# Kernel optimization log

Measured on AMD Instinct MI355X. Metric: run time of the kernel, lower is better.

## Reference

```python
import jax, jax.numpy as jnp
import numpy as np

TAU = 2.0
BN_EPS = 1e-5
SG_ALPHA = 4.0
ATTN_SCALE = 0.125
NUM_HEADS = 8
T, B, C, H, W = 2, 16, 256, 64, 64


@jax.custom_vjp
def heaviside(x):
    return (x >= 0.0).astype(x.dtype)

def _hv_fwd(x):
    return (x >= 0.0).astype(x.dtype), x

def _hv_bwd(x, g):
    s = jax.nn.sigmoid(SG_ALPHA * x)
    return (g * SG_ALPHA * s * (1.0 - s),)

heaviside.defvjp(_hv_fwd, _hv_bwd)


def lif(x_seq, v_th):
    # MultiStepLIFNode: v <- v + (x - v)/tau ; spike = H(v - v_th); hard reset to 0 (detached)
    def step(v, x):
        v = v + (x - v) / TAU
        s = heaviside(v - v_th)
        v = v * (1.0 - jax.lax.stop_gradient(s))
        return v, s
    _, spikes = jax.lax.scan(step, jnp.zeros_like(x_seq[0]), x_seq)
    return spikes


def bn1d(x, gamma, beta, mean, var):
    # eval-mode BatchNorm1d over channel axis 2 of [T,B,C,N]
    inv = (gamma / jnp.sqrt(var + BN_EPS)).reshape(1, 1, -1, 1)
    shift = (beta - mean * gamma / jnp.sqrt(var + BN_EPS)).reshape(1, 1, -1, 1)
    return x * inv + shift


def to_heads(t):
    # [T,B,C,N] -> [T,B,h,N,d]
    t_, b_, c_, n_ = t.shape
    d = c_ // NUM_HEADS
    return t.transpose(0, 1, 3, 2).reshape(t_, b_, n_, NUM_HEADS, d).transpose(0, 1, 3, 2, 4)


def setup_inputs() -> dict:
    key = jax.random.key(0)
    ks = jax.random.split(key, 24)
    w_scale = 0.06  # ~1/sqrt(C)
    inp = {
        'x': jax.random.normal(ks[0], (T, B, C, H, W), jnp.float32),
        'wq': jax.random.normal(ks[1], (C, C), jnp.float32) * w_scale,
        'wk': jax.random.normal(ks[2], (C, C), jnp.float32) * w_scale,
        'wv': jax.random.normal(ks[3], (C, C), jnp.float32) * w_scale,
        'wp': jax.random.normal(ks[4], (C, C), jnp.float32) * w_scale,
        'bp': jax.random.normal(ks[5], (C,), jnp.float32) * 0.1,
    }
    i = 6
    for p in ('q', 'k', 'v', 'p'):
        inp[p + '_gamma'] = jax.random.uniform(ks[i], (C,), jnp.float32, 0.5, 1.5); i += 1
        inp[p + '_beta'] = jax.random.normal(ks[i], (C,), jnp.float32) * 0.1; i += 1
        inp[p + '_mean'] = jax.random.normal(ks[i], (C,), jnp.float32) * 0.1; i += 1
        inp[p + '_var'] = jax.random.uniform(ks[i], (C,), jnp.float32, 0.5, 1.5); i += 1
    return inp


def reference(x, wq, wk, wv, wp, bp,
              q_gamma, q_beta, q_mean, q_var,
              k_gamma, k_beta, k_mean, k_var,
              v_gamma, v_beta, v_mean, v_var,
              p_gamma, p_beta, p_mean, p_var):
    t_, b_, c_, h_, w_ = x.shape
    n_ = h_ * w_
    xs = lif(x, 1.0).reshape(t_, b_, c_, n_)  # proj_lif then flatten(3)
    # 1x1 conv == channel matmul, then BN, then LIF (binary spikes)
    q_out = lif(bn1d(jnp.einsum('oc,tbcn->tbon', wq, xs), q_gamma, q_beta, q_mean, q_var), 1.0)
    k_out = lif(bn1d(jnp.einsum('oc,tbcn->tbon', wk, xs), k_gamma, k_beta, k_mean, k_var), 1.0)
    v_out = lif(bn1d(jnp.einsum('oc,tbcn->tbon', wv, xs), v_gamma, v_beta, v_mean, v_var), 1.0)
    q = to_heads(q_out)
    k = to_heads(k_out)
    v = to_heads(v_out)
    # linear attention: (k^T @ v) then q @ (k^T v)
    kv = jnp.einsum('tbhnd,tbhne->tbhde', k, v)  # [T,B,h,d,d]
    attn = jnp.einsum('tbhnd,tbhde->tbhne', q, kv) * ATTN_SCALE
    attn = attn.transpose(0, 1, 2, 4, 3).reshape(t_, b_, c_, n_)
    s = lif(attn, 0.5)  # attn_lif with v_threshold=0.5
    out = jnp.einsum('oc,tbcn->tbon', wp, s) + bp.reshape(1, 1, -1, 1)
    out = bn1d(out, p_gamma, p_beta, p_mean, p_var).reshape(t_, b_, c_, h_, w_)
    return (out, xs, q_out, k_out, v_out)
```

## Files before the change

### kernel.cpp

```cpp
#include <hip/hip_runtime.h>
#include <cstdint>
#include <cstddef>

typedef __attribute__((ext_vector_type(8))) short short8;
typedef __attribute__((ext_vector_type(4))) float floatx4;
typedef __attribute__((ext_vector_type(4))) unsigned int uintx4;

#define DEV static __device__ __forceinline__

constexpr int NT = 2, NB = 16, NC = 256, NN = 4096, NHD = 8;
constexpr size_t NE1 = (size_t)NT * NB * NC * NN;
constexpr size_t TSTRIDE = (size_t)NB * NC * NN;

DEV unsigned short f2bf(float x) {
  unsigned int u = __builtin_bit_cast(unsigned int, x);
  unsigned int lsb = (u >> 16) & 1u;
  u += 0x7FFFu + lsb;
  return (unsigned short)(u >> 16);
}
DEV float bfb2f(unsigned short h) {
  unsigned int u = ((unsigned int)h) << 16;
  return __builtin_bit_cast(float, u);
}
DEV unsigned int pk2(unsigned short a, unsigned short b) {
  return (unsigned int)a | ((unsigned int)b << 16);
}
DEV int swz(int fr, int kk) { return fr * 4 + (kk ^ ((fr >> 1) & 3)); }
typedef __attribute__((address_space(3))) unsigned int lds_u32;
typedef __attribute__((address_space(1))) const unsigned int glb_u32;
DEV void gld_lds16(const void* g, void* l) {
  __builtin_amdgcn_global_load_lds((glb_u32*)g, (lds_u32*)l, 16, 0, 0);
}

__global__ __launch_bounds__(256) void prep_kernel(
    const float* __restrict__ wq, const float* __restrict__ wk, const float* __restrict__ wv,
    const float* __restrict__ wp, const float* __restrict__ bp,
    const float* __restrict__ qg, const float* __restrict__ qb, const float* __restrict__ qm, const float* __restrict__ qva,
    const float* __restrict__ kg, const float* __restrict__ kb, const float* __restrict__ km, const float* __restrict__ kva,
    const float* __restrict__ vg, const float* __restrict__ vb, const float* __restrict__ vm, const float* __restrict__ vva,
    const float* __restrict__ pg, const float* __restrict__ pb, const float* __restrict__ pm, const float* __restrict__ pva,
    unsigned short* __restrict__ Wqkv, unsigned short* __restrict__ Wp,
    float* __restrict__ invqkv, float* __restrict__ shqkv,
    float* __restrict__ invp, float* __restrict__ shp)
{
  int idx = blockIdx.x * 256 + threadIdx.x;
  if (idx < 196608) {
    int o = idx >> 8, c = idx & 255;
    const float* src = (o < 256) ? wq : (o < 512) ? wk : wv;
    float w = src[(size_t)(o & 255) * 256 + c];
    unsigned short h0 = f2bf(w);  float f0 = bfb2f(h0);
    float r1 = w - f0;
    unsigned short h1 = f2bf(r1); float f1 = bfb2f(h1);
    float r2 = r1 - f1;
    unsigned short h2 = f2bf(r2);
    Wqkv[idx] = h0; Wqkv[196608 + idx] = h1; Wqkv[393216 + idx] = h2;
  } else if (idx < 262144) {
    int j = idx - 196608;
    float w = wp[j];
    unsigned short h0 = f2bf(w);  float f0 = bfb2f(h0);
    float r1 = w - f0;
    unsigned short h1 = f2bf(r1); float f1 = bfb2f(h1);
    float r2 = r1 - f1;
    unsigned short h2 = f2bf(r2);
    Wp[j] = h0; Wp[65536 + j] = h1; Wp[131072 + j] = h2;
  } else if (idx < 262912) {
    int i = idx - 262144;
    int p = i >> 8, c = i & 255;
    float g  = (p == 0) ? qg[c] : (p == 1) ? kg[c] : vg[c];
    float be = (p == 0) ? qb[c] : (p == 1) ? kb[c] : vb[c];
    float mn = (p == 0) ? qm[c] : (p == 1) ? km[c] : vm[c];
    float vr = (p == 0) ? qva[c] : (p == 1) ? kva[c] : vva[c];
    float sq = sqrtf(vr + 1e-5f);
    invqkv[i] = g / sq;
    shqkv[i]  = be - (mn * g) / sq;
  } else if (idx < 263168) {
    int c = idx - 262912;
    float sq = sqrtf(pva[c] + 1e-5f);
    float iv = pg[c] / sq;
    invp[c] = iv;
    shp[c]  = pb[c] - (pm[c] * pg[c]) / sq + bp[c] * iv;
  }
}

__global__ __launch_bounds__(256) void lifx_kernel(const float* __restrict__ x,
                                                   float* __restrict__ xs_out,
                                                   unsigned short* __restrict__ xb16)
{
  __shared__ float tile[2][64][65];
  const int nt = blockIdx.x, ct = blockIdx.y, b = blockIdx.z;
  const int tid = threadIdx.x;
  const int ci = tid >> 2, cq = tid & 3;
  const int n0 = nt * 64, c0 = ct * 64;
  const size_t rowbase = ((size_t)(b * NC + c0 + ci)) * NN + n0 + cq * 16;
  const float* px0 = x + rowbase;
  const float* px1 = x + rowbase + TSTRIDE;
  float* po0 = xs_out + rowbase;
  float* po1 = xs_out + rowbase + TSTRIDE;
  #pragma unroll
  for (int jj = 0; jj < 4; jj++) {
    floatx4 x0 = *(const floatx4*)(px0 + jj * 4);
    floatx4 x1 = *(const floatx4*)(px1 + jj * 4);
    floatx4 s0v, s1v;
    #pragma unroll
    for (int e = 0; e < 4; e++) {
      float v1 = x0[e] * 0.5f;
      float s0 = (v1 >= 1.0f) ? 1.0f : 0.0f;
      float vr = v1 * (1.0f - s0);
      float v2 = vr + (x1[e] - vr) * 0.5f;
      float s1 = (v2 >= 1.0f) ? 1.0f : 0.0f;
      s0v[e] = s0; s1v[e] = s1;
      tile[0][ci][cq * 16 + jj * 4 + e] = s0;
      tile[1][ci][cq * 16 + jj * 4 + e] = s1;
    }
    *(floatx4*)(po0 + jj * 4) = s0v;
    *(floatx4*)(po1 + jj * 4) = s1v;
  }
  __syncthreads();
  const int ni = tid >> 2, cg = tid & 3;
  #pragma unroll
  for (int t = 0; t < 2; t++) {
    unsigned int wbits = 0;
    #pragma unroll
    for (int j = 0; j < 16; j++)
      wbits |= (tile[t][cg * 16 + j][ni] != 0.f ? 1u : 0u) << j;
    xb16[((size_t)((t * NB + b) * NN) + n0 + ni) * 16 + (c0 >> 4) + cg] = (unsigned short)wbits;
  }
}

__global__ __launch_bounds__(256, 3) void qkv_gemm(
    const unsigned short* __restrict__ xb16,
    const unsigned short* __restrict__ Wsp,
    const float* __restrict__ invv, const float* __restrict__ shv,
    float* __restrict__ dq, float* __restrict__ dk, float* __restrict__ dv,
    unsigned short* __restrict__ qbits, unsigned short* __restrict__ kbits,
    unsigned short* __restrict__ vbits)
{
  __shared__ __align__(16) unsigned char smem[33280];
  unsigned short* Al = (unsigned short*)smem;
  unsigned short* Bl = (unsigned short*)(smem + 24576);
  float* yl = (float*)smem;
  const int nt = blockIdx.x, mt = blockIdx.y, b = blockIdx.z;
  const int tid = threadIdx.x;
  const int lane = tid & 63, quad = lane >> 4, l16 = lane & 15;
  const int wave = tid >> 6;
  const int tw = wave >> 1, wm = (wave & 1) * 64;
  floatx4 acc[4][4] = {};
  const int bt = tid >> 7, brow = (tid >> 1) & 63, bhalf = tid & 1;
  const unsigned short* xrow = xb16 + ((size_t)((bt * NB + b) * NN) + nt * 64 + brow) * 16 + bhalf;

  for (int k0 = 0; k0 < 256; k0 += 32) {
    __syncthreads();
    #pragma unroll
    for (int j = 0; j < 6; j++) {
      int ci = j * 256 + tid;
      int fr = ci >> 2;
      int kk = (ci & 3) ^ ((fr >> 1) & 3);
      int s = fr >> 7, row = fr & 127;
      const unsigned short* g = Wsp + (size_t)s * 196608 + (size_t)(mt * 128 + row) * 256 + k0 + kk * 8;
      gld_lds16(g, Al + (size_t)ci * 8);
    }
    {
      unsigned int wb = xrow[k0 >> 4];
      uintx4 c0v, c1v;
      #pragma unroll
      for (int p = 0; p < 4; p++) {
        c0v[p] = pk2(((wb >> (2 * p)) & 1) ? 0x3F80 : 0, ((wb >> (2 * p + 1)) & 1) ? 0x3F80 : 0);
        c1v[p] = pk2(((wb >> (8 + 2 * p)) & 1) ? 0x3F80 : 0, ((wb >> (9 + 2 * p)) & 1) ? 0x3F80 : 0);
      }
      int fr = bt * 64 + brow;
      *(uintx4*)(Bl + (size_t)swz(fr, bhalf * 2)     * 8) = c0v;
      *(uintx4*)(Bl + (size_t)swz(fr, bhalf * 2 + 1) * 8) = c1v;
    }
    __syncthreads();

    short8 bfr[4];
    #pragma unroll
    for (int ni = 0; ni < 4; ni++) {
      int fr = tw * 64 + ni * 16 + l16;
      bfr[ni] = *(const short8*)(Bl + (size_t)swz(fr, quad) * 8);
    }
    #pragma unroll
    for (int mi = 0; mi < 4; mi++) {
      const int r0 = wm + mi * 16 + l16;
      short8 a0 = *(const short8*)(Al + (size_t)swz(      r0, quad) * 8);
      short8 a1 = *(const short8*)(Al + (size_t)swz(128 + r0, quad) * 8);
      short8 a2 = *(const short8*)(Al + (size_t)swz(256 + r0, quad) * 8);
      #pragma unroll
      for (int ni = 0; ni < 4; ni++) {
        acc[mi][ni] = __builtin_amdgcn_mfma_f32_16x16x32_bf16(a0, bfr[ni], acc[mi][ni], 0, 0, 0);
        acc[mi][ni] = __builtin_amdgcn_mfma_f32_16x16x32_bf16(a1, bfr[ni], acc[mi][ni], 0, 0, 0);
        acc[mi][ni] = __builtin_amdgcn_mfma_f32_16x16x32_bf16(a2, bfr[ni], acc[mi][ni], 0, 0, 0);
      }
    }
  }
  __syncthreads();
  if (tw == 0) {
    #pragma unroll
    for (int mi = 0; mi < 4; mi++)
      #pragma unroll
      for (int r = 0; r < 4; r++)
        #pragma unroll
        for (int ni = 0; ni < 4; ni++)
          yl[(size_t)(wm + mi * 16 + quad * 4 + r) * 65 + ni * 16 + l16] = acc[mi][ni][r];
  }
  __syncthreads();
  if (tw == 1) {
    #pragma unroll
    for (int mi = 0; mi < 4; mi++) {
      #pragma unroll
      for (int r = 0; r < 4; r++) {
        const int lrow = wm + mi * 16 + quad * 4 + r;
        const int orow = mt * 128 + lrow;
        const float iv = invv[orow], sh = shv[orow];
        const int widx = orow >> 8, c = orow & 255;
        float* dst = (widx == 0) ? dq : (widx == 1) ? dk : dv;
        unsigned short* bb = (widx == 0) ? qbits : (widx == 1) ? kbits : vbits;
        #pragma unroll
        for (int ni = 0; ni < 4; ni++) {
          const int n = nt * 64 + ni * 16 + l16;
          float y0 = yl[(size_t)lrow * 65 + ni * 16 + l16] * iv + sh;
          float y1 = acc[mi][ni][r] * iv + sh;
          float v1 = y0 * 0.5f;
          float s0 = (v1 >= 1.0f) ? 1.0f : 0.0f;
          float vr = v1 * (1.0f - s0);
          float v2 = vr + (y1 - vr) * 0.5f;
          float s1 = (v2 >= 1.0f) ? 1.0f : 0.0f;
          dst[(size_t)(b * NC + c) * NN + n] = s0;
          dst[(size_t)((NB + b) * NC + c) * NN + n] = s1;
          unsigned long long bl0 = __ballot(s0 != 0.0f);
          unsigned long long bl1 = __ballot(s1 != 0.0f);
          if (l16 == 0) {
            const int w16 = nt * 4 + ni;
            bb[(size_t)b        * 65536 + (size_t)c * 256 + w16] = (unsigned short)(bl0 >> (quad * 16));
            bb[(size_t)(NB + b) * 65536 + (size_t)c * 256 + w16] = (unsigned short)(bl1 >> (quad * 16));
          }
        }
      }
    }
  }
}

__global__ __launch_bounds__(256) void kv_kernel(const unsigned long long* __restrict__ kb,
                                                 const unsigned long long* __restrict__ vb,
                                                 float* __restrict__ kvout)
{
  __shared__ unsigned long long Kl[32 * 65];
  __shared__ unsigned long long Vl[32 * 65];
  const int h = blockIdx.x, z = blockIdx.y;
  const int tid = threadIdx.x;
  for (int i = tid; i < 2048; i += 256) {
    int row = i >> 6, w = i & 63;
    size_t g = (size_t)z * 16384 + (size_t)(h * 32 + row) * 64 + w;
    Kl[row * 65 + w] = kb[g];
    Vl[row * 65 + w] = vb[g];
  }
  __syncthreads();
  const int d = tid & 31, e0 = tid >> 5;
  int acc0 = 0, acc1 = 0, acc2 = 0, acc3 = 0;
  for (int w = 0; w < 64; w++) {
    unsigned long long ku = Kl[d * 65 + w];
    acc0 += __popcll(ku & Vl[(e0     ) * 65 + w]);
    acc1 += __popcll(ku & Vl[(e0 +  8) * 65 + w]);
    acc2 += __popcll(ku & Vl[(e0 + 16) * 65 + w]);
    acc3 += __popcll(ku & Vl[(e0 + 24) * 65 + w]);
  }
  float* o = kvout + ((size_t)(z * NHD + h) << 10);
  o[d * 32 + e0     ] = (float)acc0;
  o[d * 32 + e0 +  8] = (float)acc1;
  o[d * 32 + e0 + 16] = (float)acc2;
  o[d * 32 + e0 + 24] = (float)acc3;
}

__global__ __launch_bounds__(256) void attn_kernel(const unsigned short* __restrict__ qb16,
                                                   const float* __restrict__ kvout,
                                                   unsigned short* __restrict__ sb16)
{
  __shared__ float kvl[2][32][33];
  __shared__ unsigned short qt[2][32][16];
  const int nb = blockIdx.x, h = blockIdx.y, b = blockIdx.z;
  const int tid = threadIdx.x;
  const int wave = tid >> 6, lane = tid & 63, quad = lane >> 4, l16 = lane & 15;
  for (int i = tid; i < 2048; i += 256) {
    int t = i >> 10, j = i & 1023;
    kvl[t][j >> 5][j & 31] = kvout[((size_t)((t * NB + b) * NHD + h) << 10) + j];
  }
  for (int i = tid; i < 1024; i += 256) {
    int t = i >> 9, j = i & 511, row = j >> 4, w = j & 15;
    qt[t][row][w] = qb16[(size_t)(t * NB + b) * 65536 + (size_t)(h * 32 + row) * 256 + nb * 16 + w];
  }
  __syncthreads();
  short8 bf[2][2][2];
  #pragma unroll
  for (int t = 0; t < 2; t++) {
    #pragma unroll
    for (int eh = 0; eh < 2; eh++) {
      short8 bh, bl;
      #pragma unroll
      for (int j = 0; j < 8; j++) {
        float v = kvl[t][quad * 8 + j][eh * 16 + l16];
        unsigned short h0 = f2bf(v);
        float lo = v - bfb2f(h0);
        bh[j] = (short)h0;
        bl[j] = (short)f2bf(lo);
      }
      bf[t][0][eh] = bh; bf[t][1][eh] = bl;
    }
  }
  floatx4 acc[2][4][2] = {};
  #pragma unroll
  for (int t = 0; t < 2; t++) {
    #pragma unroll
    for (int nt = 0; nt < 4; nt++) {
      const int wv = wave * 4 + nt;
      short8 af;
      #pragma unroll
      for (int j = 0; j < 8; j++) {
        unsigned short w = qt[t][quad * 8 + j][wv];
        af[j] = (short)(((w >> l16) & 1) ? 0x3F80 : 0);
      }
      #pragma unroll
      for (int eh = 0; eh < 2; eh++) {
        acc[t][nt][eh] = __builtin_amdgcn_mfma_f32_16x16x32_bf16(af, bf[t][0][eh], acc[t][nt][eh], 0, 0, 0);
        acc[t][nt][eh] = __builtin_amdgcn_mfma_f32_16x16x32_bf16(af, bf[t][1][eh], acc[t][nt][eh], 0, 0, 0);
      }
    }
  }
  const int n0 = nb * 256 + wave * 64;
  #pragma unroll
  for (int nt = 0; nt < 4; nt++) {
    #pragma unroll
    for (int r = 0; r < 4; r++) {
      const int n = n0 + nt * 16 + quad * 4 + r;
      #pragma unroll
      for (int eh = 0; eh < 2; eh++) {
        float a0 = acc[0][nt][eh][r] * 0.125f;
        float a1 = acc[1][nt][eh][r] * 0.125f;
        float v1 = a0 * 0.5f;
        float s0 = (v1 >= 0.5f) ? 1.f : 0.f;
        float vr = v1 * (1.f - s0);
        float v2 = vr + (a1 - vr) * 0.5f;
        float s1 = (v2 >= 0.5f) ? 1.f : 0.f;
        unsigned long long bl0 = __ballot(s0 != 0.f);
        unsigned long long bl1 = __ballot(s1 != 0.f);
        if (l16 == 0) {
          const int w16 = h * 2 + eh;
          sb16[(size_t)b        * 65536 + (size_t)n * 16 + w16] = (unsigned short)(bl0 >> (quad * 16));
          sb16[(size_t)(NB + b) * 65536 + (size_t)n * 16 + w16] = (unsigned short)(bl1 >> (quad * 16));
        }
      }
    }
  }
}

__global__ __launch_bounds__(256, 3) void p_gemm(
    const unsigned short* __restrict__ sb16,
    const unsigned short* __restrict__ Wsp,
    const float* __restrict__ invv, const float* __restrict__ shv,
    float* __restrict__ dout)
{
  __shared__ __align__(16) unsigned char smem[32768];
  unsigned short* Al = (unsigned short*)smem;
  unsigned short* Bl = (unsigned short*)(smem + 24576);
  const int nt = blockIdx.x, mt = blockIdx.y, z = blockIdx.z;
  const int tid = threadIdx.x;
  const int lane = tid & 63, quad = lane >> 4, l16 = lane & 15;
  const int wave = tid >> 6;
  const int wm = (wave & 1) * 64, wn = (wave >> 1) * 64;
  floatx4 acc[4][4] = {};
  const int brow = tid & 127, bhalf = tid >> 7;

  for (int k0 = 0; k0 < 256; k0 += 32) {
    __syncthreads();
    #pragma unroll
    for (int j = 0; j < 6; j++) {
      int ci = j * 256 + tid;
      int fr = ci >> 2;
      int kk = (ci & 3) ^ ((fr >> 1) & 3);
      int s = fr >> 7, row = fr & 127;
      const unsigned short* g = Wsp + (size_t)s * 65536 + (size_t)(mt * 128 + row) * 256 + k0 + kk * 8;
      gld_lds16(g, Al + (size_t)ci * 8);
    }
    {
      unsigned short wb = sb16[(size_t)z * 65536 + (size_t)(nt * 128 + brow) * 16 + (k0 >> 4) + bhalf];
      uintx4 lo4, hi4;
      #pragma unroll
      for (int p = 0; p < 4; p++) {
        lo4[p] = pk2(((wb >> (2 * p)) & 1) ? 0x3F80 : 0, ((wb >> (2 * p + 1)) & 1) ? 0x3F80 : 0);
        hi4[p] = pk2(((wb >> (8 + 2 * p)) & 1) ? 0x3F80 : 0, ((wb >> (9 + 2 * p)) & 1) ? 0x3F80 : 0);
      }
      *(uintx4*)(Bl + (size_t)swz(brow, bhalf * 2)     * 8) = lo4;
      *(uintx4*)(Bl + (size_t)swz(brow, bhalf * 2 + 1) * 8) = hi4;
    }
    __syncthreads();

    short8 bfr[4];
    #pragma unroll
    for (int ni = 0; ni < 4; ni++) {
      int fr = wn + ni * 16 + l16;
      bfr[ni] = *(const short8*)(Bl + (size_t)swz(fr, quad) * 8);
    }
    #pragma unroll
    for (int mi = 0; mi < 4; mi++) {
      const int r0 = wm + mi * 16 + l16;
      short8 a0 = *(const short8*)(Al + (size_t)swz(      r0, quad) * 8);
      short8 a1 = *(const short8*)(Al + (size_t)swz(128 + r0, quad) * 8);
      short8 a2 = *(const short8*)(Al + (size_t)swz(256 + r0, quad) * 8);
      #pragma unroll
      for (int ni = 0; ni < 4; ni++) {
        acc[mi][ni] = __builtin_amdgcn_mfma_f32_16x16x32_bf16(a0, bfr[ni], acc[mi][ni], 0, 0, 0);
        acc[mi][ni] = __builtin_amdgcn_mfma_f32_16x16x32_bf16(a1, bfr[ni], acc[mi][ni], 0, 0, 0);
        acc[mi][ni] = __builtin_amdgcn_mfma_f32_16x16x32_bf16(a2, bfr[ni], acc[mi][ni], 0, 0, 0);
      }
    }
  }
  #pragma unroll
  for (int mi = 0; mi < 4; mi++) {
    #pragma unroll
    for (int r = 0; r < 4; r++) {
      const int orow = mt * 128 + wm + mi * 16 + quad * 4 + r;
      const float iv = invv[orow], sh = shv[orow];
      #pragma unroll
      for (int ni = 0; ni < 4; ni++) {
        const int n = nt * 128 + wn + ni * 16 + l16;
        dout[((size_t)(z * NC + orow)) * NN + n] = acc[mi][ni][r] * iv + sh;
      }
    }
  }
}

extern "C" void kernel_launch(void* const* d_in, const int* in_sizes, int n_in,
                              void* d_out, int out_size, void* d_ws, size_t ws_size,
                              hipStream_t stream) {
  (void)in_sizes; (void)n_in; (void)out_size; (void)ws_size;
  const float* x  = (const float*)d_in[0];
  const float* wq = (const float*)d_in[1];
  const float* wk = (const float*)d_in[2];
  const float* wv = (const float*)d_in[3];
  const float* wp = (const float*)d_in[4];
  const float* bp = (const float*)d_in[5];
  const float* qg = (const float*)d_in[6],  *qb = (const float*)d_in[7];
  const float* qm = (const float*)d_in[8],  *qva = (const float*)d_in[9];
  const float* kg = (const float*)d_in[10], *kb = (const float*)d_in[11];
  const float* km = (const float*)d_in[12], *kva = (const float*)d_in[13];
  const float* vg = (const float*)d_in[14], *vb = (const float*)d_in[15];
  const float* vm = (const float*)d_in[16], *vva = (const float*)d_in[17];
  const float* pg = (const float*)d_in[18], *pb = (const float*)d_in[19];
  const float* pm = (const float*)d_in[20], *pva = (const float*)d_in[21];

  float* out = (float*)d_out;
  float* xs  = out + NE1;
  float* dq  = out + 2 * NE1;
  float* dk  = out + 3 * NE1;
  float* dv  = out + 4 * NE1;

  char* ws = (char*)d_ws;
  unsigned short* xbits = (unsigned short*)ws;
  unsigned short* Wqkv  = (unsigned short*)(ws + 4194304);
  unsigned short* Wp    = (unsigned short*)(ws + 5373952);
  float* kvout          = (float*)(ws + 5767168);
  unsigned short* qbits = (unsigned short*)(ws + 6815744);
  unsigned short* kbits = (unsigned short*)(ws + 11010048);
  unsigned short* vbits = (unsigned short*)(ws + 15204352);
  unsigned short* sbits = (unsigned short*)(ws + 19398656);
  float* invqkv         = (float*)(ws + 23592960);
  float* shqkv          = invqkv + 768;
  float* invp           = shqkv + 768;
  float* shp            = invp + 256;

  prep_kernel<<<1028, 256, 0, stream>>>(wq, wk, wv, wp, bp,
                                        qg, qb, qm, qva, kg, kb, km, kva,
                                        vg, vb, vm, vva, pg, pb, pm, pva,
                                        Wqkv, Wp, invqkv, shqkv, invp, shp);
  lifx_kernel<<<dim3(64, 4, 16), 256, 0, stream>>>(x, xs, xbits);
  qkv_gemm<<<dim3(64, 6, 16), 256, 0, stream>>>(xbits, Wqkv, invqkv, shqkv,
                                                dq, dk, dv, qbits, kbits, vbits);
  kv_kernel<<<dim3(8, 32), 256, 0, stream>>>((const unsigned long long*)kbits,
                                             (const unsigned long long*)vbits, kvout);
  attn_kernel<<<dim3(16, 8, 16), 256, 0, stream>>>(qbits, kvout, sbits);
  p_gemm<<<dim3(32, 2, 32), 256, 0, stream>>>(sbits, Wp, invp, shp, out);
}
```

Before: 979.8 us.

## Double-buffer LDS tiles in QKV and projection GEMMs to overlap loads with MFMA

Both GEMM kernels now keep two LDS buffers for the weight and spike-bit tiles. The next K-slice is loaded asynchronously while the current slice feeds the MFMAs, which also drops one barrier per iteration. Each thread loads its full row of spike bits into registers once up front instead of doing a small global load every iteration. LDS use doubles to 64KB and launch bounds drop from 3 to 2 blocks per CU, so occupancy falls.

New measurement: 1.001 ms. +2.1%, slower.

```diff
diff --git a/kernel.cpp b/kernel.cpp
--- a/kernel.cpp
+++ b/kernel.cpp
@@ -30,6 +30,16 @@
 typedef __attribute__((address_space(1))) const unsigned int glb_u32;
 DEV void gld_lds16(const void* g, void* l) {
   __builtin_amdgcn_global_load_lds((glb_u32*)g, (lds_u32*)l, 16, 0, 0);
+}
+DEV void stage_bits(unsigned int wb, int fr, int bhalf, unsigned short* Bdst) {
+  uintx4 c0v, c1v;
+  #pragma unroll
+  for (int p = 0; p < 4; p++) {
+    c0v[p] = pk2(((wb >> (2 * p)) & 1) ? 0x3F80 : 0, ((wb >> (2 * p + 1)) & 1) ? 0x3F80 : 0);
+    c1v[p] = pk2(((wb >> (8 + 2 * p)) & 1) ? 0x3F80 : 0, ((wb >> (9 + 2 * p)) & 1) ? 0x3F80 : 0);
+  }
+  *(uintx4*)(Bdst + (size_t)swz(fr, bhalf * 2)     * 8) = c0v;
+  *(uintx4*)(Bdst + (size_t)swz(fr, bhalf * 2 + 1) * 8) = c1v;
 }
 
 __global__ __launch_bounds__(256) void prep_kernel(
@@ -127,7 +137,7 @@
   }
 }
 
-__global__ __launch_bounds__(256, 3) void qkv_gemm(
+__global__ __launch_bounds__(256, 2) void qkv_gemm(
     const unsigned short* __restrict__ xb16,
     const unsigned short* __restrict__ Wsp,
     const float* __restrict__ invv, const float* __restrict__ shv,
@@ -135,9 +145,7 @@
     unsigned short* __restrict__ qbits, unsigned short* __restrict__ kbits,
     unsigned short* __restrict__ vbits)
 {
-  __shared__ __align__(16) unsigned char smem[33280];
-  unsigned short* Al = (unsigned short*)smem;
-  unsigned short* Bl = (unsigned short*)(smem + 24576);
+  __shared__ __align__(16) unsigned char smem[65536];
   float* yl = (float*)smem;
   const int nt = blockIdx.x, mt = blockIdx.y, b = blockIdx.z;
   const int tid = threadIdx.x;
@@ -146,45 +154,65 @@
   const int tw = wave >> 1, wm = (wave & 1) * 64;
   floatx4 acc[4][4] = {};
   const int bt = tid >> 7, brow = (tid >> 1) & 63, bhalf = tid & 1;
-  const unsigned short* xrow = xb16 + ((size_t)((bt * NB + b) * NN) + nt * 64 + brow) * 16 + bhalf;
-
-  for (int k0 = 0; k0 < 256; k0 += 32) {
-    __syncthreads();
+  const int frB = bt * 64 + brow;
+
+  const unsigned short* xrowbase = xb16 + ((size_t)((bt * NB + b) * NN) + nt * 64 + brow) * 16;
+  uintx4 xw0 = *(const uintx4*)(xrowbase);
+  uintx4 xw1 = *(const uintx4*)(xrowbase + 8);
+
+  {
     #pragma unroll
     for (int j = 0; j < 6; j++) {
       int ci = j * 256 + tid;
       int fr = ci >> 2;
       int kk = (ci & 3) ^ ((fr >> 1) & 3);
       int s = fr >> 7, row = fr & 127;
-      const unsigned short* g = Wsp + (size_t)s * 196608 + (size_t)(mt * 128 + row) * 256 + k0 + kk * 8;
-      gld_lds16(g, Al + (size_t)ci * 8);
-    }
-    {
-      unsigned int wb = xrow[k0 >> 4];
-      uintx4 c0v, c1v;
-      #pragma unroll
-      for (int p = 0; p < 4; p++) {
-        c0v[p] = pk2(((wb >> (2 * p)) & 1) ? 0x3F80 : 0, ((wb >> (2 * p + 1)) & 1) ? 0x3F80 : 0);
-        c1v[p] = pk2(((wb >> (8 + 2 * p)) & 1) ? 0x3F80 : 0, ((wb >> (9 + 2 * p)) & 1) ? 0x3F80 : 0);
-      }
-      int fr = bt * 64 + brow;
-      *(uintx4*)(Bl + (size_t)swz(fr, bhalf * 2)     * 8) = c0v;
-      *(uintx4*)(Bl + (size_t)swz(fr, bhalf * 2 + 1) * 8) = c1v;
-    }
-    __syncthreads();
+      const unsigned short* g = Wsp + (size_t)s * 196608 + (size_t)(mt * 128 + row) * 256 + 0 + kk * 8;
+      gld_lds16(g, (unsigned short*)smem + (size_t)ci * 8);
+    }
+    unsigned int w32 = xw0[0];
+    unsigned int wb = bhalf ? (w32 >> 16) : (w32 & 0xFFFFu);
+    stage_bits(wb, frB, bhalf, (unsigned short*)(smem + 49152));
+  }
+  __syncthreads();
+
+  #pragma unroll
+  for (int it = 0; it < 8; ++it) {
+    unsigned short* Ac = (unsigned short*)(smem + (it & 1) * 24576);
+    unsigned short* Bc = (unsigned short*)(smem + 49152 + (it & 1) * 8192);
+    if (it < 7) {
+      unsigned short* An = (unsigned short*)(smem + ((it + 1) & 1) * 24576);
+      const int k0 = (it + 1) * 32;
+      #pragma unroll
+      for (int j = 0; j < 6; j++) {
+        int ci = j * 256 + tid;
+        int fr = ci >> 2;
+        int kk = (ci & 3) ^ ((fr >> 1) & 3);
+        int s = fr >> 7, row = fr & 127;
+        const unsigned short* g = Wsp + (size_t)s * 196608 + (size_t)(mt * 128 + row) * 256 + k0 + kk * 8;
+        gld_lds16(g, An + (size_t)ci * 8);
+      }
+    }
+    __builtin_amdgcn_sched_barrier(0);
 
     short8 bfr[4];
     #pragma unroll
     for (int ni = 0; ni < 4; ni++) {
       int fr = tw * 64 + ni * 16 + l16;
-      bfr[ni] = *(const short8*)(Bl + (size_t)swz(fr, quad) * 8);
+      bfr[ni] = *(const short8*)(Bc + (size_t)swz(fr, quad) * 8);
+    }
+    if (it < 7) {
+      unsigned short* Bn = (unsigned short*)(smem + 49152 + (((it + 1) & 1)) * 8192);
+      unsigned int w32 = ((it + 1) < 4) ? xw0[(it + 1) & 3] : xw1[(it + 1) & 3];
+      unsigned int wb = bhalf ? (w32 >> 16) : (w32 & 0xFFFFu);
+      stage_bits(wb, frB, bhalf, Bn);
     }
     #pragma unroll
     for (int mi = 0; mi < 4; mi++) {
       const int r0 = wm + mi * 16 + l16;
-      short8 a0 = *(const short8*)(Al + (size_t)swz(      r0, quad) * 8);
-      short8 a1 = *(const short8*)(Al + (size_t)swz(128 + r0, quad) * 8);
-      short8 a2 = *(const short8*)(Al + (size_t)swz(256 + r0, quad) * 8);
+      short8 a0 = *(const short8*)(Ac + (size_t)swz(      r0, quad) * 8);
+      short8 a1 = *(const short8*)(Ac + (size_t)swz(128 + r0, quad) * 8);
+      short8 a2 = *(const short8*)(Ac + (size_t)swz(256 + r0, quad) * 8);
       #pragma unroll
       for (int ni = 0; ni < 4; ni++) {
         acc[mi][ni] = __builtin_amdgcn_mfma_f32_16x16x32_bf16(a0, bfr[ni], acc[mi][ni], 0, 0, 0);
@@ -192,8 +220,9 @@
         acc[mi][ni] = __builtin_amdgcn_mfma_f32_16x16x32_bf16(a2, bfr[ni], acc[mi][ni], 0, 0, 0);
       }
     }
-  }
-  __syncthreads();
+    __syncthreads();
+  }
+
   if (tw == 0) {
     #pragma unroll
     for (int mi = 0; mi < 4; mi++)
@@ -352,15 +381,13 @@
   }
 }
 
-__global__ __launch_bounds__(256, 3) void p_gemm(
+__global__ __launch_bounds__(256, 2) void p_gemm(
     const unsigned short* __restrict__ sb16,
     const unsigned short* __restrict__ Wsp,
     const float* __restrict__ invv, const float* __restrict__ shv,
     float* __restrict__ dout)
 {
-  __shared__ __align__(16) unsigned char smem[32768];
-  unsigned short* Al = (unsigned short*)smem;
-  unsigned short* Bl = (unsigned short*)(smem + 24576);
+  __shared__ __align__(16) unsigned char smem[65536];
   const int nt = blockIdx.x, mt = blockIdx.y, z = blockIdx.z;
   const int tid = threadIdx.x;
   const int lane = tid & 63, quad = lane >> 4, l16 = lane & 15;
@@ -369,42 +396,63 @@
   floatx4 acc[4][4] = {};
   const int brow = tid & 127, bhalf = tid >> 7;
 
-  for (int k0 = 0; k0 < 256; k0 += 32) {
-    __syncthreads();
+  const unsigned short* srowbase = sb16 + (size_t)z * 65536 + (size_t)(nt * 128 + brow) * 16;
+  uintx4 sw0 = *(const uintx4*)(srowbase);
+  uintx4 sw1 = *(const uintx4*)(srowbase + 8);
+
+  {
     #pragma unroll
     for (int j = 0; j < 6; j++) {
       int ci = j * 256 + tid;
       int fr = ci >> 2;
       int kk = (ci & 3) ^ ((fr >> 1) & 3);
       int s = fr >> 7, row = fr & 127;
-      const unsigned short* g = Wsp + (size_t)s * 65536 + (size_t)(mt * 128 + row) * 256 + k0 + kk * 8;
-      gld_lds16(g, Al + (size_t)ci * 8);
-    }
-    {
-      unsigned short wb = sb16[(size_t)z * 65536 + (size_t)(nt * 128 + brow) * 16 + (k0 >> 4) + bhalf];
-      uintx4 lo4, hi4;
-      #pragma unroll
-      for (int p = 0; p < 4; p++) {
-        lo4[p] = pk2(((wb >> (2 * p)) & 1) ? 0x3F80 : 0, ((wb >> (2 * p + 1)) & 1) ? 0x3F80 : 0);
-        hi4[p] = pk2(((wb >> (8 + 2 * p)) & 1) ? 0x3F80 : 0, ((wb >> (9 + 2 * p)) & 1) ? 0x3F80 : 0);
-      }
-      *(uintx4*)(Bl + (size_t)swz(brow, bhalf * 2)     * 8) = lo4;
-      *(uintx4*)(Bl + (size_t)swz(brow, bhalf * 2 + 1) * 8) = hi4;
-    }
-    __syncthreads();
+      const unsigned short* g = Wsp + (size_t)s * 65536 + (size_t)(mt * 128 + row) * 256 + 0 + kk * 8;
+      gld_lds16(g, (unsigned short*)smem + (size_t)ci * 8);
+    }
+    unsigned int w32 = sw0[0];
+    unsigned int wb = bhalf ? (w32 >> 16) : (w32 & 0xFFFFu);
+    stage_bits(wb, brow, bhalf, (unsigned short*)(smem + 49152));
+  }
+  __syncthreads();
+
+  #pragma unroll
+  for (int it = 0; it < 8; ++it) {
+    unsigned short* Ac = (unsigned short*)(smem + (it & 1) * 24576);
+    unsigned short* Bc = (unsigned short*)(smem + 49152 + (it & 1) * 8192);
+    if (it < 7) {
+      unsigned short* An = (unsigned short*)(smem + ((it + 1) & 1) * 24576);
+      const int k0 = (it + 1) * 32;
+      #pragma unroll
+      for (int j = 0; j < 6; j++) {
+        int ci = j * 256 + tid;
+        int fr = ci >> 2;
+        int kk = (ci & 3) ^ ((fr >> 1) & 3);
+        int s = fr >> 7, row = fr & 127;
+        const unsigned short* g = Wsp + (size_t)s * 65536 + (size_t)(mt * 128 + row) * 256 + k0 + kk * 8;
+        gld_lds16(g, An + (size_t)ci * 8);
+      }
+    }
+    __builtin_amdgcn_sched_barrier(0);
 
     short8 bfr[4];
     #pragma unroll
     for (int ni = 0; ni < 4; ni++) {
       int fr = wn + ni * 16 + l16;
-      bfr[ni] = *(const short8*)(Bl + (size_t)swz(fr, quad) * 8);
+      bfr[ni] = *(const short8*)(Bc + (size_t)swz(fr, quad) * 8);
+    }
+    if (it < 7) {
+      unsigned short* Bn = (unsigned short*)(smem + 49152 + (((it + 1) & 1)) * 8192);
+      unsigned int w32 = ((it + 1) < 4) ? sw0[(it + 1) & 3] : sw1[(it + 1) & 3];
+      unsigned int wb = bhalf ? (w32 >> 16) : (w32 & 0xFFFFu);
+      stage_bits(wb, brow, bhalf, Bn);
     }
     #pragma unroll
     for (int mi = 0; mi < 4; mi++) {
       const int r0 = wm + mi * 16 + l16;
-      short8 a0 = *(const short8*)(Al + (size_t)swz(      r0, quad) * 8);
-      short8 a1 = *(const short8*)(Al + (size_t)swz(128 + r0, quad) * 8);
-      short8 a2 = *(const short8*)(Al + (size_t)swz(256 + r0, quad) * 8);
+      short8 a0 = *(const short8*)(Ac + (size_t)swz(      r0, quad) * 8);
+      short8 a1 = *(const short8*)(Ac + (size_t)swz(128 + r0, quad) * 8);
+      short8 a2 = *(const short8*)(Ac + (size_t)swz(256 + r0, quad) * 8);
       #pragma unroll
       for (int ni = 0; ni < 4; ni++) {
         acc[mi][ni] = __builtin_amdgcn_mfma_f32_16x16x32_bf16(a0, bfr[ni], acc[mi][ni], 0, 0, 0);
@@ -412,7 +460,9 @@
         acc[mi][ni] = __builtin_amdgcn_mfma_f32_16x16x32_bf16(a2, bfr[ni], acc[mi][ni], 0, 0, 0);
       }
     }
-  }
+    __syncthreads();
+  }
+
   #pragma unroll
   for (int mi = 0; mi < 4; mi++) {
     #pragma unroll
```

## Spread QKV epilogue over all waves, hoist spike-bit loads, vectorize q-bit reads

Applied to the files above, without the earlier changes.

The QKV GEMM epilogue used to leave half the waves idle while the other half did the BatchNorm, LIF and output stores. It now stages both timesteps' accumulators into two LDS buffers over two passes, so all four waves share the store-heavy epilogue. The cost is extra barriers. Separately, both GEMMs load each row's packed spike bits once as 16-byte vectors before a fully unrolled k-loop, instead of issuing a scalar global load every iteration. The attention kernel also transposes its q-bit LDS tile so each lane reads eight words with one vector load.

Result: faster. 939.7 us (-4.1%).

```diff
diff --git a/kernel.cpp b/kernel.cpp
--- a/kernel.cpp
+++ b/kernel.cpp
@@ -30,6 +30,16 @@
 typedef __attribute__((address_space(1))) const unsigned int glb_u32;
 DEV void gld_lds16(const void* g, void* l) {
   __builtin_amdgcn_global_load_lds((glb_u32*)g, (lds_u32*)l, 16, 0, 0);
+}
+DEV void stage_bits(unsigned int wb, int fr, int bhalf, unsigned short* Bdst) {
+  uintx4 c0v, c1v;
+  #pragma unroll
+  for (int p = 0; p < 4; p++) {
+    c0v[p] = pk2(((wb >> (2 * p)) & 1) ? 0x3F80 : 0, ((wb >> (2 * p + 1)) & 1) ? 0x3F80 : 0);
+    c1v[p] = pk2(((wb >> (8 + 2 * p)) & 1) ? 0x3F80 : 0, ((wb >> (9 + 2 * p)) & 1) ? 0x3F80 : 0);
+  }
+  *(uintx4*)(Bdst + (size_t)swz(fr, bhalf * 2)     * 8) = c0v;
+  *(uintx4*)(Bdst + (size_t)swz(fr, bhalf * 2 + 1) * 8) = c1v;
 }
 
 __global__ __launch_bounds__(256) void prep_kernel(
@@ -143,12 +153,18 @@
   const int tid = threadIdx.x;
   const int lane = tid & 63, quad = lane >> 4, l16 = lane & 15;
   const int wave = tid >> 6;
-  const int tw = wave >> 1, wm = (wave & 1) * 64;
+  const int wm = (wave & 1) * 64, tw = wave >> 1;
   floatx4 acc[4][4] = {};
   const int bt = tid >> 7, brow = (tid >> 1) & 63, bhalf = tid & 1;
-  const unsigned short* xrow = xb16 + ((size_t)((bt * NB + b) * NN) + nt * 64 + brow) * 16 + bhalf;
-
-  for (int k0 = 0; k0 < 256; k0 += 32) {
+  const int frB = bt * 64 + brow;
+
+  const unsigned short* xrowbase = xb16 + ((size_t)((bt * NB + b) * NN) + nt * 64 + brow) * 16;
+  uintx4 xw0 = *(const uintx4*)(xrowbase);
+  uintx4 xw1 = *(const uintx4*)(xrowbase + 8);
+
+  #pragma unroll
+  for (int it = 0; it < 8; ++it) {
+    const int k0 = it * 32;
     __syncthreads();
     #pragma unroll
     for (int j = 0; j < 6; j++) {
@@ -160,16 +176,9 @@
       gld_lds16(g, Al + (size_t)ci * 8);
     }
     {
-      unsigned int wb = xrow[k0 >> 4];
-      uintx4 c0v, c1v;
-      #pragma unroll
-      for (int p = 0; p < 4; p++) {
-        c0v[p] = pk2(((wb >> (2 * p)) & 1) ? 0x3F80 : 0, ((wb >> (2 * p + 1)) & 1) ? 0x3F80 : 0);
-        c1v[p] = pk2(((wb >> (8 + 2 * p)) & 1) ? 0x3F80 : 0, ((wb >> (9 + 2 * p)) & 1) ? 0x3F80 : 0);
-      }
-      int fr = bt * 64 + brow;
-      *(uintx4*)(Bl + (size_t)swz(fr, bhalf * 2)     * 8) = c0v;
-      *(uintx4*)(Bl + (size_t)swz(fr, bhalf * 2 + 1) * 8) = c1v;
+      unsigned int w32 = (it < 4) ? xw0[it & 3] : xw1[it & 3];
+      unsigned int wb = bhalf ? (w32 >> 16) : (w32 & 0xFFFFu);
+      stage_bits(wb, frB, bhalf, Bl);
     }
     __syncthreads();
 
@@ -194,49 +203,52 @@
     }
   }
   __syncthreads();
-  if (tw == 0) {
-    #pragma unroll
-    for (int mi = 0; mi < 4; mi++)
-      #pragma unroll
-      for (int r = 0; r < 4; r++)
+  float* buf0 = yl;
+  float* buf1 = yl + 64 * 65;
+  #pragma unroll
+  for (int pass = 0; pass < 2; ++pass) {
+    if (wave == pass || wave == pass + 2) {
+      float* bufd = (wave == pass) ? buf0 : buf1;
+      #pragma unroll
+      for (int mi = 0; mi < 4; mi++)
         #pragma unroll
-        for (int ni = 0; ni < 4; ni++)
-          yl[(size_t)(wm + mi * 16 + quad * 4 + r) * 65 + ni * 16 + l16] = acc[mi][ni][r];
-  }
-  __syncthreads();
-  if (tw == 1) {
-    #pragma unroll
-    for (int mi = 0; mi < 4; mi++) {
-      #pragma unroll
-      for (int r = 0; r < 4; r++) {
-        const int lrow = wm + mi * 16 + quad * 4 + r;
-        const int orow = mt * 128 + lrow;
-        const float iv = invv[orow], sh = shv[orow];
-        const int widx = orow >> 8, c = orow & 255;
-        float* dst = (widx == 0) ? dq : (widx == 1) ? dk : dv;
-        unsigned short* bb = (widx == 0) ? qbits : (widx == 1) ? kbits : vbits;
-        #pragma unroll
-        for (int ni = 0; ni < 4; ni++) {
-          const int n = nt * 64 + ni * 16 + l16;
-          float y0 = yl[(size_t)lrow * 65 + ni * 16 + l16] * iv + sh;
-          float y1 = acc[mi][ni][r] * iv + sh;
-          float v1 = y0 * 0.5f;
-          float s0 = (v1 >= 1.0f) ? 1.0f : 0.0f;
-          float vr = v1 * (1.0f - s0);
-          float v2 = vr + (y1 - vr) * 0.5f;
-          float s1 = (v2 >= 1.0f) ? 1.0f : 0.0f;
-          dst[(size_t)(b * NC + c) * NN + n] = s0;
-          dst[(size_t)((NB + b) * NC + c) * NN + n] = s1;
-          unsigned long long bl0 = __ballot(s0 != 0.0f);
-          unsigned long long bl1 = __ballot(s1 != 0.0f);
-          if (l16 == 0) {
-            const int w16 = nt * 4 + ni;
-            bb[(size_t)b        * 65536 + (size_t)c * 256 + w16] = (unsigned short)(bl0 >> (quad * 16));
-            bb[(size_t)(NB + b) * 65536 + (size_t)c * 256 + w16] = (unsigned short)(bl1 >> (quad * 16));
-          }
+        for (int r = 0; r < 4; r++)
+          #pragma unroll
+          for (int ni = 0; ni < 4; ni++)
+            bufd[(size_t)(mi * 16 + quad * 4 + r) * 65 + ni * 16 + l16] = acc[mi][ni][r];
+    }
+    __syncthreads();
+    #pragma unroll
+    for (int r = 0; r < 4; r++) {
+      const int lcl = wave * 16 + quad * 4 + r;
+      const int lrow = pass * 64 + lcl;
+      const int orow = mt * 128 + lrow;
+      const float iv = invv[orow], sh = shv[orow];
+      const int widx = orow >> 8, c = orow & 255;
+      float* dst = (widx == 0) ? dq : (widx == 1) ? dk : dv;
+      unsigned short* bb = (widx == 0) ? qbits : (widx == 1) ? kbits : vbits;
+      #pragma unroll
+      for (int ni = 0; ni < 4; ni++) {
+        const int n = nt * 64 + ni * 16 + l16;
+        float y0 = buf0[(size_t)lcl * 65 + ni * 16 + l16] * iv + sh;
+        float y1 = buf1[(size_t)lcl * 65 + ni * 16 + l16] * iv + sh;
+        float v1 = y0 * 0.5f;
+        float s0 = (v1 >= 1.0f) ? 1.0f : 0.0f;
+        float vr = v1 * (1.0f - s0);
+        float v2 = vr + (y1 - vr) * 0.5f;
+        float s1 = (v2 >= 1.0f) ? 1.0f : 0.0f;
+        dst[(size_t)(b * NC + c) * NN + n] = s0;
+        dst[(size_t)((NB + b) * NC + c) * NN + n] = s1;
+        unsigned long long bl0 = __ballot(s0 != 0.0f);
+        unsigned long long bl1 = __ballot(s1 != 0.0f);
+        if (l16 == 0) {
+          const int w16 = nt * 4 + ni;
+          bb[(size_t)b        * 65536 + (size_t)c * 256 + w16] = (unsigned short)(bl0 >> (quad * 16));
+          bb[(size_t)(NB + b) * 65536 + (size_t)c * 256 + w16] = (unsigned short)(bl1 >> (quad * 16));
         }
       }
     }
+    __syncthreads();
   }
 }
 
@@ -276,7 +288,7 @@
                                                    unsigned short* __restrict__ sb16)
 {
   __shared__ float kvl[2][32][33];
-  __shared__ unsigned short qt[2][32][16];
+  __shared__ __align__(16) unsigned short qt[2][16][32];
   const int nb = blockIdx.x, h = blockIdx.y, b = blockIdx.z;
   const int tid = threadIdx.x;
   const int wave = tid >> 6, lane = tid & 63, quad = lane >> 4, l16 = lane & 15;
@@ -286,7 +298,7 @@
   }
   for (int i = tid; i < 1024; i += 256) {
     int t = i >> 9, j = i & 511, row = j >> 4, w = j & 15;
-    qt[t][row][w] = qb16[(size_t)(t * NB + b) * 65536 + (size_t)(h * 32 + row) * 256 + nb * 16 + w];
+    qt[t][w][row] = qb16[(size_t)(t * NB + b) * 65536 + (size_t)(h * 32 + row) * 256 + nb * 16 + w];
   }
   __syncthreads();
   short8 bf[2][2][2];
@@ -312,12 +324,11 @@
     #pragma unroll
     for (int nt = 0; nt < 4; nt++) {
       const int wv = wave * 4 + nt;
+      short8 qw = *(const short8*)(&qt[t][wv][quad * 8]);
       short8 af;
       #pragma unroll
-      for (int j = 0; j < 8; j++) {
-        unsigned short w = qt[t][quad * 8 + j][wv];
-        af[j] = (short)(((w >> l16) & 1) ? 0x3F80 : 0);
-      }
+      for (int j = 0; j < 8; j++)
+        af[j] = (short)((((unsigned short)qw[j] >> l16) & 1) ? 0x3F80 : 0);
       #pragma unroll
       for (int eh = 0; eh < 2; eh++) {
         acc[t][nt][eh] = __builtin_amdgcn_mfma_f32_16x16x32_bf16(af, bf[t][0][eh], acc[t][nt][eh], 0, 0, 0);
@@ -369,7 +380,13 @@
   floatx4 acc[4][4] = {};
   const int brow = tid & 127, bhalf = tid >> 7;
 
-  for (int k0 = 0; k0 < 256; k0 += 32) {
+  const unsigned short* srowbase = sb16 + (size_t)z * 65536 + (size_t)(nt * 128 + brow) * 16;
+  uintx4 sw0 = *(const uintx4*)(srowbase);
+  uintx4 sw1 = *(const uintx4*)(srowbase + 8);
+
+  #pragma unroll
+  for (int it = 0; it < 8; ++it) {
+    const int k0 = it * 32;
     __syncthreads();
     #pragma unroll
     for (int j = 0; j < 6; j++) {
@@ -381,15 +398,9 @@
       gld_lds16(g, Al + (size_t)ci * 8);
     }
     {
-      unsigned short wb = sb16[(size_t)z * 65536 + (size_t)(nt * 128 + brow) * 16 + (k0 >> 4) + bhalf];
-      uintx4 lo4, hi4;
-      #pragma unroll
-      for (int p = 0; p < 4; p++) {
-        lo4[p] = pk2(((wb >> (2 * p)) & 1) ? 0x3F80 : 0, ((wb >> (2 * p + 1)) & 1) ? 0x3F80 : 0);
-        hi4[p] = pk2(((wb >> (8 + 2 * p)) & 1) ? 0x3F80 : 0, ((wb >> (9 + 2 * p)) & 1) ? 0x3F80 : 0);
-      }
-      *(uintx4*)(Bl + (size_t)swz(brow, bhalf * 2)     * 8) = lo4;
-      *(uintx4*)(Bl + (size_t)swz(brow, bhalf * 2 + 1) * 8) = hi4;
+      unsigned int w32 = (it < 4) ? sw0[it & 3] : sw1[it & 3];
+      unsigned int wb = bhalf ? (w32 >> 16) : (w32 & 0xFFFFu);
+      stage_bits(wb, brow, bhalf, Bl);
     }
     __syncthreads();
 
```
